# Performance work log

Measured on AMD Instinct MI355X. Metric: run time of the kernel, lower is better.

The kernel has to match this reference:

```python
import jax, jax.numpy as jnp
import numpy as np

IN_CH = 128
EMBED = 64
ALPHA = 0.2  # leaky relu slope
NEG_INF = jnp.float32(-9e15)


def setup_inputs() -> dict:
    key = jax.random.key(0)
    k_x, k_adj, k_W, k_a, k_b = jax.random.split(key, 5)
    B, N = 2, 512
    x = jax.random.normal(k_x, (B, N, IN_CH), dtype=jnp.float32)
    adj = jax.random.randint(k_adj, (B, N, N), 0, 2, dtype=jnp.int32)
    # xavier_uniform with gain=1.414
    gain = 1.414
    lim_W = gain * np.sqrt(6.0 / (IN_CH + EMBED))
    W = jax.random.uniform(k_W, (IN_CH, EMBED), jnp.float32, -lim_W, lim_W)
    lim_a = gain * np.sqrt(6.0 / (2 * EMBED + 1))
    a = jax.random.uniform(k_a, (2 * EMBED, 1), jnp.float32, -lim_a, lim_a)
    bias = jax.random.normal(k_b, (EMBED,), dtype=jnp.float32) * 0.02
    return {"x": x, "adj": adj, "W": W, "a": a, "bias": bias}


def reference(x, adj, W, a, bias):
    B, N, _ = x.shape
    D = W.shape[1]
    hidden = jnp.matmul(x, W)                      # [B, N, D]
    # Faithful reproduction of the original's repeat_interleave/repeat + cat(dim=1) + view.
    chunks = jnp.repeat(hidden, N, axis=1)         # [B, N*N, D]
    alt = jnp.tile(hidden, (1, N, 1))              # [B, N*N, D]
    allc = jnp.concatenate([chunks, alt], axis=1).reshape(B, N, N, 2 * D)
    attn = jnp.matmul(allc, a)[..., 0]             # [B, N, N]
    attn = jnp.where(attn >= 0, attn, ALPHA * attn)  # leaky relu
    attn = jnp.where(adj > 0, attn, NEG_INF)
    attention = jax.nn.softmax(attn, axis=-1)
    # dropout omitted: reference is eval-mode (deterministic)
    out = jnp.matmul(attention, hidden) + bias     # [B, N, D]
    return out
```

## Files before the change

### kernel.cpp

```cpp
#include <hip/hip_runtime.h>
#include <math.h>

#define GN 512
#define GB 2
#define INCH 128
#define GD 64
#define ALPHA 0.2f
#define NEG_INF_F (-9e15f)
#define TI 4

__device__ __forceinline__ unsigned f2bf(float f) {
    unsigned u = __float_as_uint(f);
    return (u + 0x7FFFu + ((u >> 16) & 1u)) >> 16;
}
__device__ __forceinline__ float bf2f(unsigned short h) {
    return __uint_as_float(((unsigned)h) << 16);
}

__global__ __launch_bounds__(256) void k_hidden(
        const float* __restrict__ x, const float* __restrict__ W,
        const float* __restrict__ a,
        unsigned short* __restrict__ hbf, float* __restrict__ s1,
        float* __restrict__ s2) {
    const int row0 = blockIdx.x * 4;
    const int tid = threadIdx.x;
    __shared__ float Wl[INCH * GD];
    __shared__ float xs[4][INCH];

    const float4* W4 = (const float4*)W;
    float4* Wl4 = (float4*)Wl;
    #pragma unroll
    for (int t = 0; t < 8; ++t) Wl4[tid + t * 256] = W4[tid + t * 256];
    if (tid < 4 * INCH / 4)
        ((float4*)xs)[tid] = ((const float4*)(x + (size_t)row0 * INCH))[tid];
    __syncthreads();

    const int r = tid >> 6, d = tid & 63;
    float h = 0.f;
    #pragma unroll
    for (int k = 0; k < INCH; ++k) h = fmaf(xs[r][k], Wl[k * GD + d], h);
    hbf[(size_t)(row0 + r) * GD + d] = (unsigned short)f2bf(h);

    float p1 = a[d] * h, p2 = a[GD + d] * h;
    #pragma unroll
    for (int off = 32; off > 0; off >>= 1) {
        p1 += __shfl_xor(p1, off, 64);
        p2 += __shfl_xor(p2, off, 64);
    }
    if (d == 0) { s1[row0 + r] = p1; s2[row0 + r] = p2; }
}

__global__ __launch_bounds__(512) void k_attn(
        const int* __restrict__ adj, const unsigned short* __restrict__ hbf,
        const float* __restrict__ s1, const float* __restrict__ s2,
        const float* __restrict__ bias, float* __restrict__ out) {
    const int blk = blockIdx.x;
    const int b = blk >> 7;
    const int i0 = (blk & 127) * TI;
    const int tid = threadIdx.x;
    const int lane = tid & 63;
    const int w = tid >> 6;

    __shared__ float plf[GN * TI];
    __shared__ float red[8 * TI * GD];
    __shared__ float invs[TI];

    const float* s1b = s1 + b * GN;
    const float* s2b = s2 + b * GN;

    if (w < TI) {
        const int i = i0 + w;
        const int* adjw = adj + ((size_t)b * GN + i) * GN;
        float pre4[4];
        if (i < 256) {
            float c0 = s1b[2 * i] + s2b[2 * i];
            float c1 = s1b[2 * i + 1] + s2b[2 * i + 1];
            c0 = c0 >= 0.f ? c0 : ALPHA * c0;
            c1 = c1 >= 0.f ? c1 : ALPHA * c1;
            pre4[0] = pre4[1] = pre4[2] = pre4[3] = c0;
            float v[8];
            #pragma unroll
            for (int seg = 0; seg < 8; ++seg)
                v[seg] = adjw[seg * 64 + lane] > 0 ? (seg < 4 ? c0 : c1) : NEG_INF_F;
            float mx = v[0];
            #pragma unroll
            for (int seg = 1; seg < 8; ++seg) mx = fmaxf(mx, v[seg]);
            #pragma unroll
            for (int off = 32; off > 0; off >>= 1) mx = fmaxf(mx, __shfl_xor(mx, off, 64));
            float s = 0.f;
            #pragma unroll
            for (int seg = 0; seg < 8; ++seg) {
                const float e = __expf(v[seg] - mx);
                plf[(seg * 64 + lane) * TI + w] = e;
                s += e;
            }
            #pragma unroll
            for (int off = 32; off > 0; off >>= 1) s += __shfl_xor(s, off, 64);
            if (lane == 0) invs[w] = 1.f / s;
        } else {
            #pragma unroll
            for (int sg = 0; sg < 4; ++sg) {
                const int m = (sg * 64 + lane) & 255;
                float pre = s1b[2 * m] + s2b[2 * m + 1];
                pre4[sg] = pre >= 0.f ? pre : ALPHA * pre;
            }
            float v[8];
            #pragma unroll
            for (int seg = 0; seg < 8; ++seg)
                v[seg] = adjw[seg * 64 + lane] > 0 ? pre4[seg & 3] : NEG_INF_F;
            float mx = v[0];
            #pragma unroll
            for (int seg = 1; seg < 8; ++seg) mx = fmaxf(mx, v[seg]);
            #pragma unroll
            for (int off = 32; off > 0; off >>= 1) mx = fmaxf(mx, __shfl_xor(mx, off, 64));
            float s = 0.f;
            #pragma unroll
            for (int seg = 0; seg < 8; ++seg) {
                const float e = __expf(v[seg] - mx);
                plf[(seg * 64 + lane) * TI + w] = e;
                s += e;
            }
            #pragma unroll
            for (int off = 32; off > 0; off >>= 1) s += __shfl_xor(s, off, 64);
            if (lane == 0) invs[w] = 1.f / s;
        }
    }
    __syncthreads();

    const unsigned short* hbg = hbf + (size_t)b * GN * GD;
    const int j0 = w * 64;
    float o0 = 0.f, o1 = 0.f, o2 = 0.f, o3 = 0.f;
    #pragma unroll 8
    for (int jj = 0; jj < 64; ++jj) {
        const int j = j0 + jj;
        const float4 q = *((const float4*)(plf + j * TI));
        const float h = bf2f(hbg[j * GD + lane]);
        o0 = fmaf(q.x, h, o0); o1 = fmaf(q.y, h, o1);
        o2 = fmaf(q.z, h, o2); o3 = fmaf(q.w, h, o3);
    }
    red[(w * TI + 0) * GD + lane] = o0;
    red[(w * TI + 1) * GD + lane] = o1;
    red[(w * TI + 2) * GD + lane] = o2;
    red[(w * TI + 3) * GD + lane] = o3;
    __syncthreads();

    if (tid < TI * GD) {
        const int r = tid >> 6, d = tid & 63;
        float o = 0.f;
        #pragma unroll
        for (int ww = 0; ww < 8; ++ww) o += red[(ww * TI + r) * GD + d];
        o = o * invs[r] + bias[d];
        out[((size_t)b * GN + i0 + r) * GD + d] = o;
    }
}

extern "C" void kernel_launch(void* const* d_in, const int* in_sizes, int n_in,
                              void* d_out, int out_size, void* d_ws, size_t ws_size,
                              hipStream_t stream) {
    const float* x    = (const float*)d_in[0];
    const int*   adj  = (const int*)d_in[1];
    const float* W    = (const float*)d_in[2];
    const float* a    = (const float*)d_in[3];
    const float* bias = (const float*)d_in[4];
    float* out = (float*)d_out;

    unsigned short* hbf = (unsigned short*)d_ws;
    float* s1f = (float*)((char*)d_ws + GB * GN * GD * sizeof(unsigned short));
    float* s2f = s1f + GB * GN;

    k_hidden<<<GB * GN / 4, 256, 0, stream>>>(x, W, a, hbf, s1f, s2f);
    k_attn<<<GB * GN / TI, 512, 0, stream>>>(adj, hbf, s1f, s2f, bias, out);
}
```

Baseline: 15.36 us.

## Prefetch hidden rows into registers before softmax and pack bf16 pairs

```diff
diff --git a/kernel.cpp b/kernel.cpp
--- a/kernel.cpp
+++ b/kernel.cpp
@@ -60,10 +60,18 @@
     const int tid = threadIdx.x;
     const int lane = tid & 63;
     const int w = tid >> 6;
+    const int ld = lane & 31;
+    const int lh = lane >> 5;
 
     __shared__ float plf[GN * TI];
     __shared__ float red[8 * TI * GD];
-    __shared__ float invs[TI];
+
+    const unsigned short* hbg = hbf + (size_t)b * GN * GD;
+    const int j0 = w * 64;
+    unsigned int hv[32];
+    #pragma unroll
+    for (int jj = 0; jj < 32; ++jj)
+        hv[jj] = *((const unsigned int*)(hbg + (size_t)(j0 + 2 * jj + lh) * GD + 2 * ld));
 
     const float* s1b = s1 + b * GN;
     const float* s2b = s2 + b * GN;
@@ -71,77 +79,71 @@
     if (w < TI) {
         const int i = i0 + w;
         const int* adjw = adj + ((size_t)b * GN + i) * GN;
-        float pre4[4];
+        float v[8];
         if (i < 256) {
             float c0 = s1b[2 * i] + s2b[2 * i];
             float c1 = s1b[2 * i + 1] + s2b[2 * i + 1];
             c0 = c0 >= 0.f ? c0 : ALPHA * c0;
             c1 = c1 >= 0.f ? c1 : ALPHA * c1;
-            pre4[0] = pre4[1] = pre4[2] = pre4[3] = c0;
-            float v[8];
             #pragma unroll
             for (int seg = 0; seg < 8; ++seg)
                 v[seg] = adjw[seg * 64 + lane] > 0 ? (seg < 4 ? c0 : c1) : NEG_INF_F;
-            float mx = v[0];
-            #pragma unroll
-            for (int seg = 1; seg < 8; ++seg) mx = fmaxf(mx, v[seg]);
-            #pragma unroll
-            for (int off = 32; off > 0; off >>= 1) mx = fmaxf(mx, __shfl_xor(mx, off, 64));
-            float s = 0.f;
-            #pragma unroll
-            for (int seg = 0; seg < 8; ++seg) {
-                const float e = __expf(v[seg] - mx);
-                plf[(seg * 64 + lane) * TI + w] = e;
-                s += e;
-            }
-            #pragma unroll
-            for (int off = 32; off > 0; off >>= 1) s += __shfl_xor(s, off, 64);
-            if (lane == 0) invs[w] = 1.f / s;
         } else {
+            float pre4[4];
             #pragma unroll
             for (int sg = 0; sg < 4; ++sg) {
                 const int m = (sg * 64 + lane) & 255;
                 float pre = s1b[2 * m] + s2b[2 * m + 1];
                 pre4[sg] = pre >= 0.f ? pre : ALPHA * pre;
             }
-            float v[8];
             #pragma unroll
             for (int seg = 0; seg < 8; ++seg)
                 v[seg] = adjw[seg * 64 + lane] > 0 ? pre4[seg & 3] : NEG_INF_F;
-            float mx = v[0];
-            #pragma unroll
-            for (int seg = 1; seg < 8; ++seg) mx = fmaxf(mx, v[seg]);
-            #pragma unroll
-            for (int off = 32; off > 0; off >>= 1) mx = fmaxf(mx, __shfl_xor(mx, off, 64));
-            float s = 0.f;
-            #pragma unroll
-            for (int seg = 0; seg < 8; ++seg) {
-                const float e = __expf(v[seg] - mx);
-                plf[(seg * 64 + lane) * TI + w] = e;
-                s += e;
-            }
-            #pragma unroll
-            for (int off = 32; off > 0; off >>= 1) s += __shfl_xor(s, off, 64);
-            if (lane == 0) invs[w] = 1.f / s;
         }
+        float mx = v[0];
+        #pragma unroll
+        for (int seg = 1; seg < 8; ++seg) mx = fmaxf(mx, v[seg]);
+        #pragma unroll
+        for (int off = 32; off > 0; off >>= 1) mx = fmaxf(mx, __shfl_xor(mx, off, 64));
+        float e[8], s = 0.f;
+        #pragma unroll
+        for (int seg = 0; seg < 8; ++seg) {
+            e[seg] = __expf(v[seg] - mx);
+            s += e[seg];
+        }
+        #pragma unroll
+        for (int off = 32; off > 0; off >>= 1) s += __shfl_xor(s, off, 64);
+        const float inv = 1.f / s;
+        #pragma unroll
+        for (int seg = 0; seg < 8; ++seg)
+            plf[(seg * 64 + lane) * TI + w] = e[seg] * inv;
     }
     __syncthreads();
 
-    const unsigned short* hbg = hbf + (size_t)b * GN * GD;
-    const int j0 = w * 64;
-    float o0 = 0.f, o1 = 0.f, o2 = 0.f, o3 = 0.f;
+    float a00 = 0.f, a01 = 0.f, a10 = 0.f, a11 = 0.f;
+    float a20 = 0.f, a21 = 0.f, a30 = 0.f, a31 = 0.f;
     #pragma unroll 8
-    for (int jj = 0; jj < 64; ++jj) {
-        const int j = j0 + jj;
+    for (int jj = 0; jj < 32; ++jj) {
+        const int j = j0 + 2 * jj + lh;
         const float4 q = *((const float4*)(plf + j * TI));
-        const float h = bf2f(hbg[j * GD + lane]);
-        o0 = fmaf(q.x, h, o0); o1 = fmaf(q.y, h, o1);
-        o2 = fmaf(q.z, h, o2); o3 = fmaf(q.w, h, o3);
+        const float h0 = bf2f((unsigned short)(hv[jj] & 0xFFFFu));
+        const float h1 = bf2f((unsigned short)(hv[jj] >> 16));
+        a00 = fmaf(q.x, h0, a00); a01 = fmaf(q.x, h1, a01);
+        a10 = fmaf(q.y, h0, a10); a11 = fmaf(q.y, h1, a11);
+        a20 = fmaf(q.z, h0, a20); a21 = fmaf(q.z, h1, a21);
+        a30 = fmaf(q.w, h0, a30); a31 = fmaf(q.w, h1, a31);
     }
-    red[(w * TI + 0) * GD + lane] = o0;
-    red[(w * TI + 1) * GD + lane] = o1;
-    red[(w * TI + 2) * GD + lane] = o2;
-    red[(w * TI + 3) * GD + lane] = o3;
+    a00 += __shfl_xor(a00, 32, 64); a01 += __shfl_xor(a01, 32, 64);
+    a10 += __shfl_xor(a10, 32, 64); a11 += __shfl_xor(a11, 32, 64);
+    a20 += __shfl_xor(a20, 32, 64); a21 += __shfl_xor(a21, 32, 64);
+    a30 += __shfl_xor(a30, 32, 64); a31 += __shfl_xor(a31, 32, 64);
+    if (lh == 0) {
+        float2* r2 = (float2*)(red + (w * TI) * GD + 2 * ld);
+        r2[0 * GD / 2]           = make_float2(a00, a01);
+        *(float2*)(red + (w * TI + 1) * GD + 2 * ld) = make_float2(a10, a11);
+        *(float2*)(red + (w * TI + 2) * GD + 2 * ld) = make_float2(a20, a21);
+        *(float2*)(red + (w * TI + 3) * GD + 2 * ld) = make_float2(a30, a31);
+    }
     __syncthreads();
 
     if (tid < TI * GD) {
@@ -149,7 +151,7 @@
         float o = 0.f;
         #pragma unroll
         for (int ww = 0; ww < 8; ++ww) o += red[(ww * TI + r) * GD + d];
-        o = o * invs[r] + bias[d];
+        o = o + bias[d];
         out[((size_t)b * GN + i0 + r) * GD + d] = o;
     }
 }
```

Result: faster. 14.36 us (-6.5%).
